# Kernel optimization log

Hardware: AMD Instinct MI355X
Metric: run time of the kernel (lower is better)

The kernel has to match this reference:

```python
import jax, jax.numpy as jnp
import numpy as np

NUM_HEADS = 4
CATEGORY_SIZE = 128
DIM = 192
B, N, M = 2, 65000, 64


def setup_inputs() -> dict:
    key = jax.random.key(0)
    k1, k2, k3, k4 = jax.random.split(key, 4)
    qkv = jax.random.normal(k1, (B, N, 3 * DIM), dtype=jnp.float32)
    sim = jax.random.normal(k2, (B, N, M), dtype=jnp.float32)
    proj_w = jax.random.normal(k3, (DIM, DIM), dtype=jnp.float32) * (1.0 / np.sqrt(DIM))
    proj_b = jax.random.normal(k4, (DIM,), dtype=jnp.float32) * 0.01
    logit_scale = jnp.log(10.0 * jnp.ones((1, 1), dtype=jnp.float32))
    return {"qkv": qkv, "sim": sim, "proj_w": proj_w, "proj_b": proj_b,
            "logit_scale": logit_scale, "x_size": 65000}


def reference(qkv, sim, proj_w, proj_b, logit_scale, x_size):
    b, n, c3 = qkv.shape
    c = c3 // 3
    h = NUM_HEADS
    gs = min(n, CATEGORY_SIZE)
    ng = (n + gs - 1) // gs
    pad_n = ng * gs - n

    # token -> category id, then sort tokens by category
    tk_id = jnp.argmax(sim, axis=-1)                      # (b, n) int
    sort_idx = jnp.argsort(tk_id, axis=-1)                # (b, n)
    inv_idx = jnp.argsort(sort_idx, axis=-1)              # inverse permutation

    shuffled = jnp.take_along_axis(qkv, sort_idx[..., None], axis=1)  # (b, n, 3c)
    if pad_n > 0:
        pad = jnp.flip(shuffled[:, n - pad_n:n, :], axis=1)
        shuffled = jnp.concatenate([shuffled, pad], axis=1)           # (b, n+pad_n, 3c)

    # (3, b, ng, h, gs, c/h)
    y = shuffled.reshape(b, ng, gs, 3, h, c // h).transpose(3, 0, 1, 4, 2, 5)
    q, k, v = y[0], y[1], y[2]

    scale = jnp.exp(jnp.minimum(logit_scale, jnp.log(jnp.asarray(100.0, dtype=qkv.dtype))))
    attn = jnp.einsum('bghqd,bghkd->bghqk', q, k) * scale  # (b, ng, h, gs, gs)
    attn = jax.nn.softmax(attn, axis=-1)
    out = jnp.einsum('bghqk,bghkd->bghqd', attn, v)        # (b, ng, h, gs, c/h)
    out = out.transpose(0, 1, 3, 2, 4).reshape(b, n + pad_n, c)[:, :n, :]

    # scatter back to original token order
    out = jnp.take_along_axis(out, inv_idx[..., None], axis=1)
    return out @ proj_w.T + proj_b
```

## Files before the change

### kernel.cpp

```cpp
#include <hip/hip_runtime.h>
#include <hip/hip_bf16.h>
#include <math.h>

#define BB 2
#define NN 65000
#define MM 64
#define DIM 192
#define NH 4
#define HD 48
#define GS 128
#define NG 508
#define SORT_TPB 256
#define NBLK 254

#define NROWS_PAD 130048
#define NROWTILES 2032

typedef __attribute__((ext_vector_type(8))) short bf16x8;
typedef __attribute__((ext_vector_type(8))) _Float16 f16x8;
typedef __attribute__((ext_vector_type(2))) __fp16 fp16x2;
typedef __attribute__((ext_vector_type(4))) float f32x4;
typedef __attribute__((ext_vector_type(16))) float f32x16;
typedef __attribute__((ext_vector_type(8))) unsigned short u16x8;

__device__ __forceinline__ unsigned short f2bf(float f) {
  __hip_bfloat16 h = __float2bfloat16(f);
  return *(unsigned short*)&h;
}
__device__ __forceinline__ unsigned int pkh(float lo, float hi) {
  fp16x2 t = __builtin_amdgcn_cvt_pkrtz(lo, hi);
  return *(unsigned int*)&t;
}
__device__ __forceinline__ f16x8 cvt8h(float4 a, float4 b) {
  f16x8 r;
  r[0] = (_Float16)a.x; r[1] = (_Float16)a.y; r[2] = (_Float16)a.z; r[3] = (_Float16)a.w;
  r[4] = (_Float16)b.x; r[5] = (_Float16)b.y; r[6] = (_Float16)b.z; r[7] = (_Float16)b.w;
  return r;
}
__device__ __forceinline__ void gload_lds16(const float* src, float* lds_dst) {
  __builtin_amdgcn_global_load_lds(
      (const __attribute__((address_space(1))) unsigned int*)src,
      (__attribute__((address_space(3))) unsigned int*)lds_dst, 16, 0, 0);
}

__global__ void k_argmax_hist(const float* __restrict__ sim, int* __restrict__ tk,
                              int* __restrict__ hist) {
  __shared__ int cnt[MM];
  const int b = blockIdx.y, blk = blockIdx.x;
  if (threadIdx.x < MM) cnt[threadIdx.x] = 0;
  __syncthreads();
  int t = blk * SORT_TPB + threadIdx.x;
  if (t < NN) {
    const float4* row = (const float4*)(sim + ((size_t)b * NN + t) * MM);
    float best = -INFINITY;
    int bi = 0;
#pragma unroll
    for (int j = 0; j < MM / 4; ++j) {
      float4 v = row[j];
      if (v.x > best) { best = v.x; bi = 4 * j + 0; }
      if (v.y > best) { best = v.y; bi = 4 * j + 1; }
      if (v.z > best) { best = v.z; bi = 4 * j + 2; }
      if (v.w > best) { best = v.w; bi = 4 * j + 3; }
    }
    tk[b * NN + t] = bi;
    atomicAdd(&cnt[bi], 1);
  }
  __syncthreads();
  if (threadIdx.x < MM)
    hist[(b * NBLK + blk) * MM + threadIdx.x] = cnt[threadIdx.x];
}

__global__ void k_scan(const int* __restrict__ hist, int* __restrict__ boff) {
  const int b = blockIdx.x;
  const int tid = threadIdx.x;
  const int seg = tid >> 6, bin = tid & 63;
  __shared__ int part[4][MM];
  __shared__ int basev[MM];
  const int lo = seg * 64, hi = (seg == 3) ? NBLK : (lo + 64);
  int s = 0;
  for (int blk = lo; blk < hi; ++blk) s += hist[(b * NBLK + blk) * MM + bin];
  part[seg][bin] = s;
  __syncthreads();
  if (tid < 64) {
    int tot = part[0][bin] + part[1][bin] + part[2][bin] + part[3][bin];
    int incl = tot;
#pragma unroll
    for (int d = 1; d < 64; d <<= 1) {
      int o = __shfl_up(incl, d);
      if (bin >= d) incl += o;
    }
    basev[bin] = incl - tot;
  }
  __syncthreads();
  int run = basev[bin];
  for (int s2 = 0; s2 < seg; ++s2) run += part[s2][bin];
  for (int blk = lo; blk < hi; ++blk) {
    int h = hist[(b * NBLK + blk) * MM + bin];
    boff[(b * NBLK + blk) * MM + bin] = run;
    run += h;
  }
}

__global__ void k_scatter(const int* __restrict__ tk, const int* __restrict__ boff,
                          int* __restrict__ sidx) {
  __shared__ int whist[4][MM];
  const int b = blockIdx.y, blk = blockIdx.x;
  const int tid = threadIdx.x;
  const int w = tid >> 6, lane = tid & 63;
  ((int*)whist)[tid] = 0;
  __syncthreads();
  int t = blk * SORT_TPB + tid;
  int bin = (t < NN) ? tk[b * NN + t] : -1;
  unsigned long long m = ~0ull;
#pragma unroll
  for (int bit = 0; bit < 6; ++bit) {
    unsigned long long bl = __ballot((bin >> bit) & 1);
    m &= ((bin >> bit) & 1) ? bl : ~bl;
  }
  int rank_w = __popcll(m & ((1ull << lane) - 1ull));
  if (bin >= 0 && rank_w == 0) whist[w][bin] = __popcll(m);
  __syncthreads();
  if (bin >= 0) {
    int rank = rank_w;
#pragma unroll
    for (int w2 = 0; w2 < 3; ++w2)
      if (w2 < w) rank += whist[w2][bin];
    int pos = boff[(b * NBLK + blk) * MM + bin] + rank;
    sidx[b * NN + pos] = t;
  }
}

__global__ __launch_bounds__(256, 4) void k_attn_mfma(const float* __restrict__ qkv,
                                                      const int* __restrict__ sidx,
                                                      const float* __restrict__ logit_scale,
                                                      __hip_bfloat16* __restrict__ attn_out) {
  const int x = blockIdx.x;
  const int g = ((x >> 5) << 3) + (x & 7);
  const int hd = (x >> 3) & 3;
  const int b = blockIdx.z;
  if (g >= NG) return;

  __shared__ int stok[GS];
  __shared__ __align__(16) _Float16 akv[4 * 3 * 64 * 8];
  __shared__ __align__(16) _Float16 vfrag[2 * 8 * 64 * 8];

  const int tid = threadIdx.x;
  const int w = tid >> 6, l = tid & 63;
  const int hl = l >> 5, l31 = l & 31;

  if (tid < GS) {
    int s = g * GS + tid;
    int sp = (s < NN) ? s : (2 * NN - 1 - s);
    stok[tid] = sidx[b * NN + sp];
  }
  __syncthreads();

#pragma unroll
  for (int i = 0; i < 3; ++i) {
    int c = tid + 256 * i;
    int ts = c >> 6, cl = c & 63;
    int kvr = (ts / 3) * 32 + (cl & 31);
    int dbase = (ts % 3) * 16 + (cl >> 5) * 8;
    const float* src = qkv + (size_t)(b * NN + stok[kvr]) * (3 * DIM) + DIM + hd * HD + dbase;
    ((f16x8*)akv)[c] = cvt8h(((const float4*)src)[0], ((const float4*)src)[1]);
  }

#pragma unroll
  for (int i = 0; i < 4; ++i) {
    int c = tid + 256 * i;
    int ntks = c >> 6, cl = c & 63;
    int nt = ntks >> 3, ks = ntks & 7;
    int d = nt * 32 + (cl & 31);
    int kvb = ks * 16 + (cl >> 5) * 8;
    _Float16 tmp[8];
    if (d < HD) {
#pragma unroll
      for (int e = 0; e < 8; ++e)
        tmp[e] = (_Float16)qkv[(size_t)(b * NN + stok[kvb + e]) * (3 * DIM) + 2 * DIM + hd * HD + d];
    } else {
#pragma unroll
      for (int e = 0; e < 8; ++e) tmp[e] = (_Float16)0.f;
    }
    ((f16x8*)vfrag)[c] = *(f16x8*)tmp;
  }

  f16x8 qf[3];
  {
    const float* qsrc = qkv + (size_t)(b * NN + stok[w * 32 + l31]) * (3 * DIM) + hd * HD;
#pragma unroll
    for (int s = 0; s < 3; ++s) {
      const float4* p = (const float4*)(qsrc + s * 16 + hl * 8);
      qf[s] = cvt8h(p[0], p[1]);
    }
  }
  __syncthreads();

  f32x16 accS[4];
#pragma unroll
  for (int t = 0; t < 4; ++t)
#pragma unroll
    for (int r = 0; r < 16; ++r) accS[t][r] = 0.f;

#pragma unroll
  for (int t = 0; t < 4; ++t)
#pragma unroll
    for (int s = 0; s < 3; ++s) {
      f16x8 af = ((const f16x8*)akv)[(t * 3 + s) * 64 + l];
      accS[t] = __builtin_amdgcn_mfma_f32_32x32x16_f16(af, qf[s], accS[t], 0, 0, 0);
    }

  const float scale = expf(fminf(logit_scale[0], 4.6051701860f));
  float mx = -INFINITY;
#pragma unroll
  for (int t = 0; t < 4; ++t)
#pragma unroll
    for (int r = 0; r < 16; ++r) { accS[t][r] *= scale; mx = fmaxf(mx, accS[t][r]); }
  mx = fmaxf(mx, __shfl_xor(mx, 32));
  float sum = 0.f;
#pragma unroll
  for (int t = 0; t < 4; ++t)
#pragma unroll
    for (int r = 0; r < 16; ++r) { float p = __expf(accS[t][r] - mx); accS[t][r] = p; sum += p; }
  sum += __shfl_xor(sum, 32);
  const float inv = 1.f / sum;
#pragma unroll
  for (int t = 0; t < 4; ++t)
#pragma unroll
    for (int r = 0; r < 16; ++r) accS[t][r] *= inv;

  f32x16 accO[2];
#pragma unroll
  for (int nt = 0; nt < 2; ++nt)
#pragma unroll
    for (int r = 0; r < 16; ++r) accO[nt][r] = 0.f;

#pragma unroll
  for (int t = 0; t < 4; ++t) {
    union { unsigned int u[4]; f16x8 v; } fa, fb;
    {
      unsigned int a0 = pkh(accS[t][0], accS[t][1]);
      unsigned int a1 = pkh(accS[t][2], accS[t][3]);
      unsigned int b0 = pkh(accS[t][4], accS[t][5]);
      unsigned int b1 = pkh(accS[t][6], accS[t][7]);
      unsigned int sa0 = __shfl_xor(a0, 32), sa1 = __shfl_xor(a1, 32);
      unsigned int sb0 = __shfl_xor(b0, 32), sb1 = __shfl_xor(b1, 32);
      fa.u[0] = hl ? sb0 : a0; fa.u[1] = hl ? sb1 : a1;
      fa.u[2] = hl ? b0 : sa0; fa.u[3] = hl ? b1 : sa1;
    }
    {
      unsigned int a0 = pkh(accS[t][8], accS[t][9]);
      unsigned int a1 = pkh(accS[t][10], accS[t][11]);
      unsigned int b0 = pkh(accS[t][12], accS[t][13]);
      unsigned int b1 = pkh(accS[t][14], accS[t][15]);
      unsigned int sa0 = __shfl_xor(a0, 32), sa1 = __shfl_xor(a1, 32);
      unsigned int sb0 = __shfl_xor(b0, 32), sb1 = __shfl_xor(b1, 32);
      fb.u[0] = hl ? sb0 : a0; fb.u[1] = hl ? sb1 : a1;
      fb.u[2] = hl ? b0 : sa0; fb.u[3] = hl ? b1 : sa1;
    }
    accO[0] = __builtin_amdgcn_mfma_f32_32x32x16_f16(fa.v, ((const f16x8*)vfrag)[(0 * 8 + 2 * t) * 64 + l], accO[0], 0, 0, 0);
    accO[1] = __builtin_amdgcn_mfma_f32_32x32x16_f16(fa.v, ((const f16x8*)vfrag)[(1 * 8 + 2 * t) * 64 + l], accO[1], 0, 0, 0);
    accO[0] = __builtin_amdgcn_mfma_f32_32x32x16_f16(fb.v, ((const f16x8*)vfrag)[(0 * 8 + 2 * t + 1) * 64 + l], accO[0], 0, 0, 0);
    accO[1] = __builtin_amdgcn_mfma_f32_32x32x16_f16(fb.v, ((const f16x8*)vfrag)[(1 * 8 + 2 * t + 1) * 64 + l], accO[1], 0, 0, 0);
  }

#pragma unroll
  for (int r = 0; r < 16; ++r) {
    int rowl = w * 32 + (r & 3) + 8 * (r >> 2) + 4 * hl;
    int sg = g * GS + rowl;
    if (sg < NN) {
      size_t base = (size_t)(b * NN + stok[rowl]) * DIM + hd * HD;
      attn_out[base + l31] = __float2bfloat16(accO[0][r]);
      if (l31 < 16) attn_out[base + 32 + l31] = __float2bfloat16(accO[1][r]);
    }
  }
}

__global__ void k_wpack(const float* __restrict__ W, unsigned short* __restrict__ wpack) {
  int idx = blockIdx.x * blockDim.x + threadIdx.x;
  if (idx >= 12 * 6 * 64) return;
  int lane = idx & 63;
  int kkjt = idx >> 6;
  int kk = kkjt % 6;
  int jt = kkjt / 6;
  int j = jt * 16 + (lane & 15);
  int k0 = kk * 32 + (lane >> 4) * 8;
  const float* src = W + (size_t)j * DIM + k0;
  unsigned short tmp[8];
#pragma unroll
  for (int e = 0; e < 8; ++e) tmp[e] = f2bf(src[e]);
  ((u16x8*)wpack)[idx] = *(const u16x8*)tmp;
}

__global__ __launch_bounds__(256) void k_proj_mfma(const unsigned short* __restrict__ xb,
                                                   const unsigned short* __restrict__ wpack,
                                                   const float* __restrict__ bias,
                                                   float* __restrict__ out) {
  __shared__ unsigned short wl[12 * 6 * 64 * 8];
  const int tid = threadIdx.x;

#pragma unroll
  for (int j = 0; j < 18; ++j) {
    int c = j * 256 + tid;
    gload_lds16((const float*)((const u16x8*)wpack + c), (float*)((u16x8*)wl + c));
  }

  const int wid = tid >> 6, lane = tid & 63;
  const int l15 = lane & 15, lk = lane >> 4;

  float bv[12];
#pragma unroll
  for (int jt = 0; jt < 12; ++jt) bv[jt] = bias[jt * 16 + l15];

  __syncthreads();

  for (int tile = blockIdx.x; tile < NROWTILES; tile += gridDim.x) {
    const int r0 = tile * 64 + wid * 16;
    f32x4 acc[12];
#pragma unroll
    for (int jt = 0; jt < 12; ++jt) { f32x4 t = {bv[jt], bv[jt], bv[jt], bv[jt]}; acc[jt] = t; }

    const unsigned short* xrow = xb + (size_t)(r0 + l15) * DIM;
#pragma unroll
    for (int kk = 0; kk < 6; ++kk) {
      bf16x8 a = *(const bf16x8*)(xrow + kk * 32 + lk * 8);
#pragma unroll
      for (int jt = 0; jt < 12; ++jt) {
        bf16x8 b = *(const bf16x8*)(wl + ((jt * 6 + kk) * 64 + lane) * 8);
        acc[jt] = __builtin_amdgcn_mfma_f32_16x16x32_bf16(a, b, acc[jt], 0, 0, 0);
      }
    }

    const int rowb = r0 + lk * 4;
#pragma unroll
    for (int jt = 0; jt < 12; ++jt) {
#pragma unroll
      for (int r = 0; r < 4; ++r) {
        int row = rowb + r;
        if (row < BB * NN)
          out[(size_t)row * DIM + jt * 16 + l15] = acc[jt][r];
      }
    }
  }
}

extern "C" void kernel_launch(void* const* d_in, const int* in_sizes, int n_in,
                              void* d_out, int out_size, void* d_ws, size_t ws_size,
                              hipStream_t stream) {
  const float* qkv = (const float*)d_in[0];
  const float* sim = (const float*)d_in[1];
  const float* proj_w = (const float*)d_in[2];
  const float* proj_b = (const float*)d_in[3];
  const float* logit_scale = (const float*)d_in[4];

  unsigned short* x_bf16 = (unsigned short*)d_ws;
  unsigned short* wpack = x_bf16 + (size_t)NROWS_PAD * DIM;
  int* tk = (int*)(wpack + 12 * 6 * 64 * 8);
  int* hist = tk + (size_t)BB * NN;
  int* boff = hist + (size_t)BB * NBLK * MM;
  int* sidx = boff + (size_t)BB * NBLK * MM;

  k_argmax_hist<<<dim3(NBLK, BB), SORT_TPB, 0, stream>>>(sim, tk, hist);
  k_scan<<<BB, 256, 0, stream>>>(hist, boff);
  k_scatter<<<dim3(NBLK, BB), SORT_TPB, 0, stream>>>(tk, boff, sidx);
  k_wpack<<<(12 * 6 * 64 + 255) / 256, 256, 0, stream>>>(proj_w, wpack);
  k_attn_mfma<<<dim3(2048, 1, BB), 256, 0, stream>>>(qkv, sidx, logit_scale,
                                                     (__hip_bfloat16*)x_bf16);
  k_proj_mfma<<<dim3(1016), 256, 0, stream>>>(x_bf16, wpack, proj_b, (float*)d_out);
}
```

Before: 162.5 us.

## Write attention output in sorted order and scatter after projection; two heads per block

The attention kernel now writes its bf16 output contiguously in sorted-token order instead of scattering each row to the original token position. The projection kernel then reads those rows sequentially and uses sidx to scatter the fp32 results back to original order. Each attention block also handles two heads, which halves the grid and reuses the loaded token index list. The scan kernel uses 1024 threads with 16 segments to shorten each thread's serial loop. The costs are roughly double the LDS per attention block, which may lower occupancy, and scattered fp32 stores of full 768-byte rows in the projection kernel.

Result: slower. 171.0 us (+5.2%).

```diff
diff --git a/kernel.cpp b/kernel.cpp
--- a/kernel.cpp
+++ b/kernel.cpp
@@ -13,8 +13,8 @@
 #define SORT_TPB 256
 #define NBLK 254
 
-#define NROWS_PAD 130048
-#define NROWTILES 2032
+#define XROWS 65024
+#define XTILES_B 1016
 
 typedef __attribute__((ext_vector_type(8))) short bf16x8;
 typedef __attribute__((ext_vector_type(8))) _Float16 f16x8;
@@ -70,19 +70,24 @@
     hist[(b * NBLK + blk) * MM + threadIdx.x] = cnt[threadIdx.x];
 }
 
+#define SEGS 16
+#define SEGB 16
 __global__ void k_scan(const int* __restrict__ hist, int* __restrict__ boff) {
   const int b = blockIdx.x;
   const int tid = threadIdx.x;
   const int seg = tid >> 6, bin = tid & 63;
-  __shared__ int part[4][MM];
+  __shared__ int part[SEGS][MM];
   __shared__ int basev[MM];
-  const int lo = seg * 64, hi = (seg == 3) ? NBLK : (lo + 64);
+  const int lo = seg * SEGB;
+  const int hi = min(NBLK, lo + SEGB);
   int s = 0;
   for (int blk = lo; blk < hi; ++blk) s += hist[(b * NBLK + blk) * MM + bin];
   part[seg][bin] = s;
   __syncthreads();
   if (tid < 64) {
-    int tot = part[0][bin] + part[1][bin] + part[2][bin] + part[3][bin];
+    int tot = 0;
+#pragma unroll
+    for (int s2 = 0; s2 < SEGS; ++s2) tot += part[s2][bin];
     int incl = tot;
 #pragma unroll
     for (int d = 1; d < 64; d <<= 1) {
@@ -130,19 +135,20 @@
   }
 }
 
-__global__ __launch_bounds__(256, 4) void k_attn_mfma(const float* __restrict__ qkv,
-                                                      const int* __restrict__ sidx,
-                                                      const float* __restrict__ logit_scale,
-                                                      __hip_bfloat16* __restrict__ attn_out) {
+__global__ __launch_bounds__(256) void k_attn_mfma(const float* __restrict__ qkv,
+                                                   const int* __restrict__ sidx,
+                                                   const float* __restrict__ logit_scale,
+                                                   __hip_bfloat16* __restrict__ attn_out) {
   const int x = blockIdx.x;
-  const int g = ((x >> 5) << 3) + (x & 7);
-  const int hd = (x >> 3) & 3;
+  const int g = ((x >> 4) << 3) + (x & 7);
+  const int p = (x >> 3) & 1;
   const int b = blockIdx.z;
   if (g >= NG) return;
+  const int hd0 = 2 * p;
 
   __shared__ int stok[GS];
-  __shared__ __align__(16) _Float16 akv[4 * 3 * 64 * 8];
-  __shared__ __align__(16) _Float16 vfrag[2 * 8 * 64 * 8];
+  __shared__ __align__(16) _Float16 akv2[2][4 * 3 * 64 * 8];
+  __shared__ __align__(16) _Float16 vfrag2[2][2 * 8 * 64 * 8];
 
   const int tid = threadIdx.x;
   const int w = tid >> 6, l = tid & 63;
@@ -156,121 +162,132 @@
   __syncthreads();
 
 #pragma unroll
-  for (int i = 0; i < 3; ++i) {
-    int c = tid + 256 * i;
-    int ts = c >> 6, cl = c & 63;
-    int kvr = (ts / 3) * 32 + (cl & 31);
-    int dbase = (ts % 3) * 16 + (cl >> 5) * 8;
-    const float* src = qkv + (size_t)(b * NN + stok[kvr]) * (3 * DIM) + DIM + hd * HD + dbase;
-    ((f16x8*)akv)[c] = cvt8h(((const float4*)src)[0], ((const float4*)src)[1]);
-  }
-
-#pragma unroll
-  for (int i = 0; i < 4; ++i) {
-    int c = tid + 256 * i;
-    int ntks = c >> 6, cl = c & 63;
-    int nt = ntks >> 3, ks = ntks & 7;
-    int d = nt * 32 + (cl & 31);
-    int kvb = ks * 16 + (cl >> 5) * 8;
-    _Float16 tmp[8];
-    if (d < HD) {
-#pragma unroll
-      for (int e = 0; e < 8; ++e)
-        tmp[e] = (_Float16)qkv[(size_t)(b * NN + stok[kvb + e]) * (3 * DIM) + 2 * DIM + hd * HD + d];
-    } else {
-#pragma unroll
-      for (int e = 0; e < 8; ++e) tmp[e] = (_Float16)0.f;
-    }
-    ((f16x8*)vfrag)[c] = *(f16x8*)tmp;
-  }
-
-  f16x8 qf[3];
+  for (int head = 0; head < 2; ++head)
+#pragma unroll
+    for (int i = 0; i < 3; ++i) {
+      int cc = tid + 256 * i;
+      int ts = cc >> 6, cl = cc & 63;
+      int kvr = (ts / 3) * 32 + (cl & 31);
+      int dbase = (ts % 3) * 16 + (cl >> 5) * 8;
+      const float* src = qkv + (size_t)(b * NN + stok[kvr]) * (3 * DIM) + DIM + (hd0 + head) * HD + dbase;
+      ((f16x8*)akv2[head])[cc] = cvt8h(((const float4*)src)[0], ((const float4*)src)[1]);
+    }
+
+#pragma unroll
+  for (int head = 0; head < 2; ++head)
+#pragma unroll
+    for (int i = 0; i < 4; ++i) {
+      int cc = tid + 256 * i;
+      int ntks = cc >> 6, cl = cc & 63;
+      int nt = ntks >> 3, ks = ntks & 7;
+      int d = nt * 32 + (cl & 31);
+      int kvb = ks * 16 + (cl >> 5) * 8;
+      _Float16 tmp[8];
+      if (d < HD) {
+#pragma unroll
+        for (int e = 0; e < 8; ++e)
+          tmp[e] = (_Float16)qkv[(size_t)(b * NN + stok[kvb + e]) * (3 * DIM) + 2 * DIM + (hd0 + head) * HD + d];
+      } else {
+#pragma unroll
+        for (int e = 0; e < 8; ++e) tmp[e] = (_Float16)0.f;
+      }
+      ((f16x8*)vfrag2[head])[cc] = *(f16x8*)tmp;
+    }
+
+  f16x8 qf[2][3];
   {
-    const float* qsrc = qkv + (size_t)(b * NN + stok[w * 32 + l31]) * (3 * DIM) + hd * HD;
-#pragma unroll
-    for (int s = 0; s < 3; ++s) {
-      const float4* p = (const float4*)(qsrc + s * 16 + hl * 8);
-      qf[s] = cvt8h(p[0], p[1]);
-    }
-  }
-  __syncthreads();
-
-  f32x16 accS[4];
-#pragma unroll
-  for (int t = 0; t < 4; ++t)
-#pragma unroll
-    for (int r = 0; r < 16; ++r) accS[t][r] = 0.f;
-
-#pragma unroll
-  for (int t = 0; t < 4; ++t)
-#pragma unroll
-    for (int s = 0; s < 3; ++s) {
-      f16x8 af = ((const f16x8*)akv)[(t * 3 + s) * 64 + l];
-      accS[t] = __builtin_amdgcn_mfma_f32_32x32x16_f16(af, qf[s], accS[t], 0, 0, 0);
-    }
+    const float* qb = qkv + (size_t)(b * NN + stok[w * 32 + l31]) * (3 * DIM);
+#pragma unroll
+    for (int head = 0; head < 2; ++head)
+#pragma unroll
+      for (int s = 0; s < 3; ++s) {
+        const float4* ptr = (const float4*)(qb + (hd0 + head) * HD + s * 16 + hl * 8);
+        qf[head][s] = cvt8h(ptr[0], ptr[1]);
+      }
+  }
+  __syncthreads();
 
   const float scale = expf(fminf(logit_scale[0], 4.6051701860f));
-  float mx = -INFINITY;
-#pragma unroll
-  for (int t = 0; t < 4; ++t)
-#pragma unroll
-    for (int r = 0; r < 16; ++r) { accS[t][r] *= scale; mx = fmaxf(mx, accS[t][r]); }
-  mx = fmaxf(mx, __shfl_xor(mx, 32));
-  float sum = 0.f;
-#pragma unroll
-  for (int t = 0; t < 4; ++t)
-#pragma unroll
-    for (int r = 0; r < 16; ++r) { float p = __expf(accS[t][r] - mx); accS[t][r] = p; sum += p; }
-  sum += __shfl_xor(sum, 32);
-  const float inv = 1.f / sum;
-#pragma unroll
-  for (int t = 0; t < 4; ++t)
-#pragma unroll
-    for (int r = 0; r < 16; ++r) accS[t][r] *= inv;
-
-  f32x16 accO[2];
-#pragma unroll
-  for (int nt = 0; nt < 2; ++nt)
-#pragma unroll
-    for (int r = 0; r < 16; ++r) accO[nt][r] = 0.f;
-
-#pragma unroll
-  for (int t = 0; t < 4; ++t) {
-    union { unsigned int u[4]; f16x8 v; } fa, fb;
-    {
-      unsigned int a0 = pkh(accS[t][0], accS[t][1]);
-      unsigned int a1 = pkh(accS[t][2], accS[t][3]);
-      unsigned int b0 = pkh(accS[t][4], accS[t][5]);
-      unsigned int b1 = pkh(accS[t][6], accS[t][7]);
-      unsigned int sa0 = __shfl_xor(a0, 32), sa1 = __shfl_xor(a1, 32);
-      unsigned int sb0 = __shfl_xor(b0, 32), sb1 = __shfl_xor(b1, 32);
-      fa.u[0] = hl ? sb0 : a0; fa.u[1] = hl ? sb1 : a1;
-      fa.u[2] = hl ? b0 : sa0; fa.u[3] = hl ? b1 : sa1;
-    }
-    {
-      unsigned int a0 = pkh(accS[t][8], accS[t][9]);
-      unsigned int a1 = pkh(accS[t][10], accS[t][11]);
-      unsigned int b0 = pkh(accS[t][12], accS[t][13]);
-      unsigned int b1 = pkh(accS[t][14], accS[t][15]);
-      unsigned int sa0 = __shfl_xor(a0, 32), sa1 = __shfl_xor(a1, 32);
-      unsigned int sb0 = __shfl_xor(b0, 32), sb1 = __shfl_xor(b1, 32);
-      fb.u[0] = hl ? sb0 : a0; fb.u[1] = hl ? sb1 : a1;
-      fb.u[2] = hl ? b0 : sa0; fb.u[3] = hl ? b1 : sa1;
-    }
-    accO[0] = __builtin_amdgcn_mfma_f32_32x32x16_f16(fa.v, ((const f16x8*)vfrag)[(0 * 8 + 2 * t) * 64 + l], accO[0], 0, 0, 0);
-    accO[1] = __builtin_amdgcn_mfma_f32_32x32x16_f16(fa.v, ((const f16x8*)vfrag)[(1 * 8 + 2 * t) * 64 + l], accO[1], 0, 0, 0);
-    accO[0] = __builtin_amdgcn_mfma_f32_32x32x16_f16(fb.v, ((const f16x8*)vfrag)[(0 * 8 + 2 * t + 1) * 64 + l], accO[0], 0, 0, 0);
-    accO[1] = __builtin_amdgcn_mfma_f32_32x32x16_f16(fb.v, ((const f16x8*)vfrag)[(1 * 8 + 2 * t + 1) * 64 + l], accO[1], 0, 0, 0);
-  }
-
-#pragma unroll
-  for (int r = 0; r < 16; ++r) {
-    int rowl = w * 32 + (r & 3) + 8 * (r >> 2) + 4 * hl;
-    int sg = g * GS + rowl;
-    if (sg < NN) {
-      size_t base = (size_t)(b * NN + stok[rowl]) * DIM + hd * HD;
-      attn_out[base + l31] = __float2bfloat16(accO[0][r]);
-      if (l31 < 16) attn_out[base + 32 + l31] = __float2bfloat16(accO[1][r]);
+
+  for (int hh = 0; hh < 2; ++hh) {
+    const int hd = hd0 + hh;
+
+    f32x16 accS[4];
+#pragma unroll
+    for (int t = 0; t < 4; ++t)
+#pragma unroll
+      for (int r = 0; r < 16; ++r) accS[t][r] = 0.f;
+
+#pragma unroll
+    for (int t = 0; t < 4; ++t)
+#pragma unroll
+      for (int s = 0; s < 3; ++s) {
+        f16x8 af = ((const f16x8*)akv2[hh])[(t * 3 + s) * 64 + l];
+        accS[t] = __builtin_amdgcn_mfma_f32_32x32x16_f16(af, qf[hh][s], accS[t], 0, 0, 0);
+      }
+
+    float mx = -INFINITY;
+#pragma unroll
+    for (int t = 0; t < 4; ++t)
+#pragma unroll
+      for (int r = 0; r < 16; ++r) { accS[t][r] *= scale; mx = fmaxf(mx, accS[t][r]); }
+    mx = fmaxf(mx, __shfl_xor(mx, 32));
+    float sum = 0.f;
+#pragma unroll
+    for (int t = 0; t < 4; ++t)
+#pragma unroll
+      for (int r = 0; r < 16; ++r) { float pv = __expf(accS[t][r] - mx); accS[t][r] = pv; sum += pv; }
+    sum += __shfl_xor(sum, 32);
+    const float inv = 1.f / sum;
+#pragma unroll
+    for (int t = 0; t < 4; ++t)
+#pragma unroll
+      for (int r = 0; r < 16; ++r) accS[t][r] *= inv;
+
+    f32x16 accO[2];
+#pragma unroll
+    for (int nt = 0; nt < 2; ++nt)
+#pragma unroll
+      for (int r = 0; r < 16; ++r) accO[nt][r] = 0.f;
+
+#pragma unroll
+    for (int t = 0; t < 4; ++t) {
+      union { unsigned int u[4]; f16x8 v; } fa, fb;
+      {
+        unsigned int a0 = pkh(accS[t][0], accS[t][1]);
+        unsigned int a1 = pkh(accS[t][2], accS[t][3]);
+        unsigned int b0 = pkh(accS[t][4], accS[t][5]);
+        unsigned int b1 = pkh(accS[t][6], accS[t][7]);
+        unsigned int sa0 = __shfl_xor(a0, 32), sa1 = __shfl_xor(a1, 32);
+        unsigned int sb0 = __shfl_xor(b0, 32), sb1 = __shfl_xor(b1, 32);
+        fa.u[0] = hl ? sb0 : a0; fa.u[1] = hl ? sb1 : a1;
+        fa.u[2] = hl ? b0 : sa0; fa.u[3] = hl ? b1 : sa1;
+      }
+      {
+        unsigned int a0 = pkh(accS[t][8], accS[t][9]);
+        unsigned int a1 = pkh(accS[t][10], accS[t][11]);
+        unsigned int b0 = pkh(accS[t][12], accS[t][13]);
+        unsigned int b1 = pkh(accS[t][14], accS[t][15]);
+        unsigned int sa0 = __shfl_xor(a0, 32), sa1 = __shfl_xor(a1, 32);
+        unsigned int sb0 = __shfl_xor(b0, 32), sb1 = __shfl_xor(b1, 32);
+        fb.u[0] = hl ? sb0 : a0; fb.u[1] = hl ? sb1 : a1;
+        fb.u[2] = hl ? b0 : sa0; fb.u[3] = hl ? b1 : sa1;
+      }
+      accO[0] = __builtin_amdgcn_mfma_f32_32x32x16_f16(fa.v, ((const f16x8*)vfrag2[hh])[(0 * 8 + 2 * t) * 64 + l], accO[0], 0, 0, 0);
+      accO[1] = __builtin_amdgcn_mfma_f32_32x32x16_f16(fa.v, ((const f16x8*)vfrag2[hh])[(1 * 8 + 2 * t) * 64 + l], accO[1], 0, 0, 0);
+      accO[0] = __builtin_amdgcn_mfma_f32_32x32x16_f16(fb.v, ((const f16x8*)vfrag2[hh])[(0 * 8 + 2 * t + 1) * 64 + l], accO[0], 0, 0, 0);
+      accO[1] = __builtin_amdgcn_mfma_f32_32x32x16_f16(fb.v, ((const f16x8*)vfrag2[hh])[(1 * 8 + 2 * t + 1) * 64 + l], accO[1], 0, 0, 0);
+    }
+
+#pragma unroll
+    for (int r = 0; r < 16; ++r) {
+      int rowl = w * 32 + (r & 3) + 8 * (r >> 2) + 4 * hl;
+      int sg = g * GS + rowl;
+      if (sg < NN) {
+        size_t base = ((size_t)b * XROWS + sg) * DIM + hd * HD;
+        attn_out[base + l31] = __float2bfloat16(accO[0][r]);
+        if (l31 < 16) attn_out[base + 32 + l31] = __float2bfloat16(accO[1][r]);
+      }
     }
   }
 }
@@ -292,6 +309,7 @@
 }
 
 __global__ __launch_bounds__(256) void k_proj_mfma(const unsigned short* __restrict__ xb,
+                                                   const int* __restrict__ sidx,
                                                    const unsigned short* __restrict__ wpack,
                                                    const float* __restrict__ bias,
                                                    float* __restrict__ out) {
@@ -313,31 +331,36 @@
 
   __syncthreads();
 
-  for (int tile = blockIdx.x; tile < NROWTILES; tile += gridDim.x) {
-    const int r0 = tile * 64 + wid * 16;
+  for (int tile = blockIdx.x; tile < BB * XTILES_B; tile += gridDim.x) {
+    const int b = tile / XTILES_B;
+    const int r0 = (tile % XTILES_B) * 64 + wid * 16;
     f32x4 acc[12];
 #pragma unroll
     for (int jt = 0; jt < 12; ++jt) { f32x4 t = {bv[jt], bv[jt], bv[jt], bv[jt]}; acc[jt] = t; }
 
-    const unsigned short* xrow = xb + (size_t)(r0 + l15) * DIM;
+    const unsigned short* xrow = xb + ((size_t)b * XROWS + r0 + l15) * DIM;
 #pragma unroll
     for (int kk = 0; kk < 6; ++kk) {
       bf16x8 a = *(const bf16x8*)(xrow + kk * 32 + lk * 8);
 #pragma unroll
       for (int jt = 0; jt < 12; ++jt) {
-        bf16x8 b = *(const bf16x8*)(wl + ((jt * 6 + kk) * 64 + lane) * 8);
-        acc[jt] = __builtin_amdgcn_mfma_f32_16x16x32_bf16(a, b, acc[jt], 0, 0, 0);
+        bf16x8 bfr = *(const bf16x8*)(wl + ((jt * 6 + kk) * 64 + lane) * 8);
+        acc[jt] = __builtin_amdgcn_mfma_f32_16x16x32_bf16(a, bfr, acc[jt], 0, 0, 0);
       }
     }
 
     const int rowb = r0 + lk * 4;
+    int orow[4];
+#pragma unroll
+    for (int r = 0; r < 4; ++r)
+      orow[r] = (rowb + r < NN) ? sidx[b * NN + rowb + r] : -1;
+
 #pragma unroll
     for (int jt = 0; jt < 12; ++jt) {
 #pragma unroll
       for (int r = 0; r < 4; ++r) {
-        int row = rowb + r;
-        if (row < BB * NN)
-          out[(size_t)row * DIM + jt * 16 + l15] = acc[jt][r];
+        if (orow[r] >= 0)
+          out[((size_t)b * NN + orow[r]) * DIM + jt * 16 + l15] = acc[jt][r];
       }
     }
   }
@@ -353,17 +376,17 @@
   const float* logit_scale = (const float*)d_in[4];
 
   unsigned short* x_bf16 = (unsigned short*)d_ws;
-  unsigned short* wpack = x_bf16 + (size_t)NROWS_PAD * DIM;
+  unsigned short* wpack = x_bf16 + (size_t)BB * XROWS * DIM;
   int* tk = (int*)(wpack + 12 * 6 * 64 * 8);
   int* hist = tk + (size_t)BB * NN;
   int* boff = hist + (size_t)BB * NBLK * MM;
   int* sidx = boff + (size_t)BB * NBLK * MM;
 
   k_argmax_hist<<<dim3(NBLK, BB), SORT_TPB, 0, stream>>>(sim, tk, hist);
-  k_scan<<<BB, 256, 0, stream>>>(hist, boff);
+  k_scan<<<BB, 1024, 0, stream>>>(hist, boff);
   k_scatter<<<dim3(NBLK, BB), SORT_TPB, 0, stream>>>(tk, boff, sidx);
   k_wpack<<<(12 * 6 * 64 + 255) / 256, 256, 0, stream>>>(proj_w, wpack);
-  k_attn_mfma<<<dim3(2048, 1, BB), 256, 0, stream>>>(qkv, sidx, logit_scale,
+  k_attn_mfma<<<dim3(1024, 1, BB), 256, 0, stream>>>(qkv, sidx, logit_scale,
                                                      (__hip_bfloat16*)x_bf16);
-  k_proj_mfma<<<dim3(1016), 256, 0, stream>>>(x_bf16, wpack, proj_b, (float*)d_out);
-}
+  k_proj_mfma<<<dim3(1016), 256, 0, stream>>>(x_bf16, sidx, wpack, proj_b, (float*)d_out);
+}
```

## Write attention output in sorted order and scatter in projection epilogue

Applied to the files above, without the earlier changes.

The attention kernel now writes its bf16 output contiguously in sorted-group order instead of scattering each row to its original token position. The projection kernel reads these contiguous rows and applies the inverse permutation when storing the fp32 output, loading sidx per row. The scan kernel is widened to 1024 threads with 16 segments, and the occupancy hint on the attention kernel is dropped. This moves the scattered writes from bf16 rows to fp32 rows, where each row is stored as 16-wide column pieces per wavefront, which may change coalescing.

Measured after the change: 161.5 us. No clear change (-0.6%).

```diff
diff --git a/kernel.cpp b/kernel.cpp
--- a/kernel.cpp
+++ b/kernel.cpp
@@ -13,8 +13,8 @@
 #define SORT_TPB 256
 #define NBLK 254
 
-#define NROWS_PAD 130048
-#define NROWTILES 2032
+#define XROWS 65024
+#define XTILES_B 1016
 
 typedef __attribute__((ext_vector_type(8))) short bf16x8;
 typedef __attribute__((ext_vector_type(8))) _Float16 f16x8;
@@ -70,19 +70,24 @@
     hist[(b * NBLK + blk) * MM + threadIdx.x] = cnt[threadIdx.x];
 }
 
+#define SEGS 16
+#define SEGB 16
 __global__ void k_scan(const int* __restrict__ hist, int* __restrict__ boff) {
   const int b = blockIdx.x;
   const int tid = threadIdx.x;
   const int seg = tid >> 6, bin = tid & 63;
-  __shared__ int part[4][MM];
+  __shared__ int part[SEGS][MM];
   __shared__ int basev[MM];
-  const int lo = seg * 64, hi = (seg == 3) ? NBLK : (lo + 64);
+  const int lo = seg * SEGB;
+  const int hi = min(NBLK, lo + SEGB);
   int s = 0;
   for (int blk = lo; blk < hi; ++blk) s += hist[(b * NBLK + blk) * MM + bin];
   part[seg][bin] = s;
   __syncthreads();
   if (tid < 64) {
-    int tot = part[0][bin] + part[1][bin] + part[2][bin] + part[3][bin];
+    int tot = 0;
+#pragma unroll
+    for (int s2 = 0; s2 < SEGS; ++s2) tot += part[s2][bin];
     int incl = tot;
 #pragma unroll
     for (int d = 1; d < 64; d <<= 1) {
@@ -130,10 +135,10 @@
   }
 }
 
-__global__ __launch_bounds__(256, 4) void k_attn_mfma(const float* __restrict__ qkv,
-                                                      const int* __restrict__ sidx,
-                                                      const float* __restrict__ logit_scale,
-                                                      __hip_bfloat16* __restrict__ attn_out) {
+__global__ __launch_bounds__(256) void k_attn_mfma(const float* __restrict__ qkv,
+                                                   const int* __restrict__ sidx,
+                                                   const float* __restrict__ logit_scale,
+                                                   __hip_bfloat16* __restrict__ attn_out) {
   const int x = blockIdx.x;
   const int g = ((x >> 5) << 3) + (x & 7);
   const int hd = (x >> 3) & 3;
@@ -268,7 +273,7 @@
     int rowl = w * 32 + (r & 3) + 8 * (r >> 2) + 4 * hl;
     int sg = g * GS + rowl;
     if (sg < NN) {
-      size_t base = (size_t)(b * NN + stok[rowl]) * DIM + hd * HD;
+      size_t base = ((size_t)b * XROWS + sg) * DIM + hd * HD;
       attn_out[base + l31] = __float2bfloat16(accO[0][r]);
       if (l31 < 16) attn_out[base + 32 + l31] = __float2bfloat16(accO[1][r]);
     }
@@ -292,6 +297,7 @@
 }
 
 __global__ __launch_bounds__(256) void k_proj_mfma(const unsigned short* __restrict__ xb,
+                                                   const int* __restrict__ sidx,
                                                    const unsigned short* __restrict__ wpack,
                                                    const float* __restrict__ bias,
                                                    float* __restrict__ out) {
@@ -313,31 +319,36 @@
 
   __syncthreads();
 
-  for (int tile = blockIdx.x; tile < NROWTILES; tile += gridDim.x) {
-    const int r0 = tile * 64 + wid * 16;
+  for (int tile = blockIdx.x; tile < BB * XTILES_B; tile += gridDim.x) {
+    const int b = tile / XTILES_B;
+    const int r0 = (tile % XTILES_B) * 64 + wid * 16;
     f32x4 acc[12];
 #pragma unroll
     for (int jt = 0; jt < 12; ++jt) { f32x4 t = {bv[jt], bv[jt], bv[jt], bv[jt]}; acc[jt] = t; }
 
-    const unsigned short* xrow = xb + (size_t)(r0 + l15) * DIM;
+    const unsigned short* xrow = xb + ((size_t)b * XROWS + r0 + l15) * DIM;
 #pragma unroll
     for (int kk = 0; kk < 6; ++kk) {
       bf16x8 a = *(const bf16x8*)(xrow + kk * 32 + lk * 8);
 #pragma unroll
       for (int jt = 0; jt < 12; ++jt) {
-        bf16x8 b = *(const bf16x8*)(wl + ((jt * 6 + kk) * 64 + lane) * 8);
-        acc[jt] = __builtin_amdgcn_mfma_f32_16x16x32_bf16(a, b, acc[jt], 0, 0, 0);
+        bf16x8 bfr = *(const bf16x8*)(wl + ((jt * 6 + kk) * 64 + lane) * 8);
+        acc[jt] = __builtin_amdgcn_mfma_f32_16x16x32_bf16(a, bfr, acc[jt], 0, 0, 0);
       }
     }
 
     const int rowb = r0 + lk * 4;
+    int orow[4];
+#pragma unroll
+    for (int r = 0; r < 4; ++r)
+      orow[r] = (rowb + r < NN) ? sidx[b * NN + rowb + r] : -1;
+
 #pragma unroll
     for (int jt = 0; jt < 12; ++jt) {
 #pragma unroll
       for (int r = 0; r < 4; ++r) {
-        int row = rowb + r;
-        if (row < BB * NN)
-          out[(size_t)row * DIM + jt * 16 + l15] = acc[jt][r];
+        if (orow[r] >= 0)
+          out[((size_t)b * NN + orow[r]) * DIM + jt * 16 + l15] = acc[jt][r];
       }
     }
   }
@@ -353,17 +364,17 @@
   const float* logit_scale = (const float*)d_in[4];
 
   unsigned short* x_bf16 = (unsigned short*)d_ws;
-  unsigned short* wpack = x_bf16 + (size_t)NROWS_PAD * DIM;
+  unsigned short* wpack = x_bf16 + (size_t)BB * XROWS * DIM;
   int* tk = (int*)(wpack + 12 * 6 * 64 * 8);
   int* hist = tk + (size_t)BB * NN;
   int* boff = hist + (size_t)BB * NBLK * MM;
   int* sidx = boff + (size_t)BB * NBLK * MM;
 
   k_argmax_hist<<<dim3(NBLK, BB), SORT_TPB, 0, stream>>>(sim, tk, hist);
-  k_scan<<<BB, 256, 0, stream>>>(hist, boff);
+  k_scan<<<BB, 1024, 0, stream>>>(hist, boff);
   k_scatter<<<dim3(NBLK, BB), SORT_TPB, 0, stream>>>(tk, boff, sidx);
   k_wpack<<<(12 * 6 * 64 + 255) / 256, 256, 0, stream>>>(proj_w, wpack);
   k_attn_mfma<<<dim3(2048, 1, BB), 256, 0, stream>>>(qkv, sidx, logit_scale,
                                                      (__hip_bfloat16*)x_bf16);
-  k_proj_mfma<<<dim3(1016), 256, 0, stream>>>(x_bf16, wpack, proj_b, (float*)d_out);
-}
+  k_proj_mfma<<<dim3(1016), 256, 0, stream>>>(x_bf16, sidx, wpack, proj_b, (float*)d_out);
+}
```
